# Kernel optimization log

Measured on AMD Instinct MI355X. Metric: run time of the kernel, lower is better.

The kernel has to match this reference:

```python
import jax, jax.numpy as jnp
import numpy as np

B, A, F, D, C = 256, 128, 512, 6, 512  # batch, max_atoms, atom_features, max_degree, conv_width


def setup_inputs() -> dict:
    key = jax.random.key(0)
    k1, k2, k3, k4 = jax.random.split(key, 4)
    atoms = jax.random.normal(k1, (B, A, F), dtype=jnp.float32)
    # neighbour indices in [0, A); pad entries beyond each atom's degree with -1
    neigh = jax.random.randint(k2, (B, A, D), 0, A)
    deg = jax.random.randint(k3, (B, A, 1), 0, D)  # degrees in 0..D-1
    bonds = jnp.where(jnp.arange(D)[None, None, :] < deg, neigh, -1)
    # one Dense(conv_width) per degree: stacked kernels [D, F, C] and biases [D, C]
    W = jax.random.normal(k4, (D, F, C), dtype=jnp.float32) * 0.02
    b = jnp.zeros((D, C), dtype=jnp.float32)
    return {"atoms": atoms, "bonds": bonds, "W": W, "b": b}


def reference(atoms, bonds, W, b):
    d_max = bonds.shape[-1]
    # per-atom degree = count of non -1 neighbour slots  [B, A, 1]
    degrees = jnp.sum(bonds != -1, axis=-1, keepdims=True)
    # shift lookup by 1 so that padded (-1) neighbours index a zero row
    padded = jnp.pad(atoms, ((0, 0), (1, 1), (0, 0)))  # [B, A+2, F]
    idx = bonds + 1  # [B, A, D]
    # per-sample gather of neighbour features -> [B, A, D, F]
    neigh_feats = jax.vmap(lambda ref, i: ref[i])(padded, idx)
    summed = jnp.sum(neigh_feats, axis=2) + atoms  # [B, A, F]
    # apply all degree-specific dense layers, then mask-select by degree
    dense = jnp.einsum('baf,dfc->badc', summed, W) + b  # [B, A, D, C]
    masks = (degrees[..., None] == jnp.arange(d_max).reshape(1, 1, d_max, 1)).astype(dense.dtype)
    return jnp.sum(dense * masks, axis=2)  # [B, A, C]
```

## Files before the change

kernel.cpp:

```cpp
#include <hip/hip_runtime.h>
#include <hip/hip_bf16.h>


#define NB 256
#define NA 128
#define NF 512
#define ND 6
#define NC 512
#define NATOMS (NB * NA)

typedef __attribute__((ext_vector_type(8))) short frag8;
typedef __attribute__((ext_vector_type(4))) float f32x4;

static __device__ inline unsigned short f2bu(float f) {
    __hip_bfloat16 h = __float2bfloat16(f);
    return *reinterpret_cast<unsigned short*>(&h);
}
static __device__ inline unsigned int pack2(float a, float b) {
    return (unsigned int)f2bu(a) | ((unsigned int)f2bu(b) << 16);
}
static __device__ inline void async16(const void* g, void* l) {
    __builtin_amdgcn_global_load_lds(
        (const __attribute__((address_space(1))) void*)g,
        (__attribute__((address_space(3))) void*)l, 16, 0, 0);
}

__global__ void transpose_w(const float* __restrict__ W,
                            __hip_bfloat16* __restrict__ Wt,
                            int* __restrict__ counts) {
    if (blockIdx.x == 0 && blockIdx.y == 0 && blockIdx.z == 0 &&
        threadIdx.y == 0 && threadIdx.x < ND)
        counts[threadIdx.x] = 0;
    __shared__ float t[32][33];
    const int d  = blockIdx.z;
    const int c0 = blockIdx.x * 32;
    const int f0 = blockIdx.y * 32;
    #pragma unroll
    for (int r = 0; r < 32; r += 8)
        t[threadIdx.y + r][threadIdx.x] =
            W[((size_t)(d * NF + f0 + threadIdx.y + r)) * NC + c0 + threadIdx.x];
    __syncthreads();
    #pragma unroll
    for (int r = 0; r < 32; r += 8)
        Wt[((size_t)(d * NC + c0 + threadIdx.y + r)) * NF + f0 + threadIdx.x] =
            __float2bfloat16(t[threadIdx.x][threadIdx.y + r]);
}

__global__ __launch_bounds__(256) void bucket_atoms(
    const int* __restrict__ bonds, int* __restrict__ counts,
    int* __restrict__ bucket) {
    __shared__ int lcnt[ND];
    __shared__ int lbase[ND];
    const int tid = threadIdx.x;
    if (tid < ND) lcnt[tid] = 0;
    __syncthreads();
    int deg[4], loc[4], gg[4];
    #pragma unroll
    for (int i = 0; i < 4; ++i) {
        int g = blockIdx.x * 1024 + i * 256 + tid;
        gg[i] = g;
        int dg = 0;
        #pragma unroll
        for (int j = 0; j < ND; ++j) dg += (bonds[g * ND + j] >= 0);
        deg[i] = dg;
        loc[i] = atomicAdd(&lcnt[dg], 1);
    }
    __syncthreads();
    if (tid < ND) lbase[tid] = atomicAdd(&counts[tid], lcnt[tid]);
    __syncthreads();
    #pragma unroll
    for (int i = 0; i < 4; ++i)
        bucket[deg[i] * NATOMS + lbase[deg[i]] + loc[i]] = gg[i];
}

__global__ __launch_bounds__(256) void sum_neigh(
    const float* __restrict__ atoms, const int* __restrict__ bonds,
    __hip_bfloat16* __restrict__ summed) {
    const int tid  = threadIdx.x;
    const int wave = tid >> 6;
    const int lane = tid & 63;
    const int swz  = (blockIdx.x & 7) * (NATOMS / 4 / 8) + (blockIdx.x >> 3);
    const int g    = swz * 4 + wave;
    const float4* a4 = (const float4*)atoms;

    int   nb[ND];
    float msk[ND];
    #pragma unroll
    for (int j = 0; j < ND; ++j) {
        int n = bonds[g * ND + j];
        msk[j] = (n >= 0) ? 1.0f : 0.0f;
        nb[j]  = (n >= 0) ? n : 0;
    }
    const int rowbase = g & ~(NA - 1);

    float4 s0 = a4[(size_t)g * 128 + lane];
    float4 s1 = a4[(size_t)g * 128 + 64 + lane];
    float4 v0[ND], v1[ND];
    #pragma unroll
    for (int j = 0; j < ND; ++j) {
        const size_t base = (size_t)(rowbase + nb[j]) * 128;
        v0[j] = a4[base + lane];
        v1[j] = a4[base + 64 + lane];
    }
    #pragma unroll
    for (int j = 0; j < ND; ++j) {
        s0.x = fmaf(v0[j].x, msk[j], s0.x); s0.y = fmaf(v0[j].y, msk[j], s0.y);
        s0.z = fmaf(v0[j].z, msk[j], s0.z); s0.w = fmaf(v0[j].w, msk[j], s0.w);
        s1.x = fmaf(v1[j].x, msk[j], s1.x); s1.y = fmaf(v1[j].y, msk[j], s1.y);
        s1.z = fmaf(v1[j].z, msk[j], s1.z); s1.w = fmaf(v1[j].w, msk[j], s1.w);
    }

    uint2 o0, o1;
    o0.x = pack2(s0.x, s0.y); o0.y = pack2(s0.z, s0.w);
    o1.x = pack2(s1.x, s1.y); o1.y = pack2(s1.z, s1.w);
    ((uint2*)summed)[(size_t)g * 128 + lane] = o0;
    ((uint2*)summed)[(size_t)g * 128 + 64 + lane] = o1;
}

__global__ __launch_bounds__(256, 2) void gemm_deg(
    const __hip_bfloat16* __restrict__ summed, const __hip_bfloat16* __restrict__ Wt,
    const float* __restrict__ bias, const int* __restrict__ counts,
    const int* __restrict__ bucket, float* __restrict__ out) {
    const int L  = blockIdx.x + 24 * blockIdx.y;
    const int q  = L >> 3;
    const int p  = ((q >> 2) << 3) + (L & 7);
    const int d  = p % ND;
    const int m0 = (p / ND) * 128;
    const int n0 = (q & 3) * 128;
    const int Md = counts[d];
    if (m0 >= Md) return;

    __shared__ __align__(16) __hip_bfloat16 sA[2][128 * 64];
    __shared__ __align__(16) __hip_bfloat16 sB[2][128 * 64];
    __shared__ int sRows[128];

    const int tid = threadIdx.x;
    if (tid < 128) {
        int r = m0 + tid;
        sRows[tid] = (r < Md) ? bucket[d * NATOMS + r] : -1;
    }
    __syncthreads();

    const int lane = tid & 63;
    const int w    = tid >> 6;
    const int srow = lane >> 3;
    const int seg  = lane & 7;

    const char* smB = (const char*)summed;
    const char* wtB = (const char*)Wt + (size_t)(d * NC + n0) * (NF * 2);
    size_t gA[4];
    int    rowc[4];
    #pragma unroll
    for (int c = 0; c < 4; ++c) {
        rowc[c] = w * 32 + c * 8 + srow;
        int qr = sRows[rowc[c]];
        gA[c] = (size_t)((qr < 0) ? 0 : qr) * (NF * 2);
    }

    const int quad = lane >> 4, l16 = lane & 15;
    const int wy = w >> 1, wx = w & 1;

    f32x4 acc[4][4];
    #pragma unroll
    for (int i = 0; i < 4; ++i)
        #pragma unroll
        for (int j = 0; j < 4; ++j) acc[i][j] = (f32x4)0.0f;

    auto stage = [&](int buf, int kt) {
        const int koff = kt * 128 + seg * 16;
        #pragma unroll
        for (int c = 0; c < 4; ++c) {
            async16(smB + gA[c] + koff, &sA[buf][(w * 32 + c * 8) * 64]);
            async16(wtB + (size_t)rowc[c] * (NF * 2) + koff, &sB[buf][(w * 32 + c * 8) * 64]);
        }
    };
    auto compute = [&](int buf) {
        #pragma unroll
        for (int ks = 0; ks < 64; ks += 32) {
            frag8 aF[4], bF[4];
            #pragma unroll
            for (int i = 0; i < 4; ++i)
                aF[i] = *(const frag8*)&sA[buf][(wy * 64 + i * 16 + l16) * 64 + ks + quad * 8];
            #pragma unroll
            for (int j = 0; j < 4; ++j)
                bF[j] = *(const frag8*)&sB[buf][(wx * 64 + j * 16 + l16) * 64 + ks + quad * 8];
            #pragma unroll
            for (int i = 0; i < 4; ++i)
                #pragma unroll
                for (int j = 0; j < 4; ++j)
                    acc[i][j] = __builtin_amdgcn_mfma_f32_16x16x32_bf16(
                        aF[i], bF[j], acc[i][j], 0, 0, 0);
        }
    };

    stage(0, 0);
    __syncthreads();
    int cur = 0;
    #pragma unroll
    for (int kt = 1; kt < NF / 64; ++kt) {
        stage(cur ^ 1, kt);
        compute(cur);
        __syncthreads();
        cur ^= 1;
    }
    compute(cur);

    #pragma unroll
    for (int j = 0; j < 4; ++j) {
        const int n = n0 + wx * 64 + j * 16 + l16;
        const float bv = bias[d * NC + n];
        #pragma unroll
        for (int i = 0; i < 4; ++i) {
            #pragma unroll
            for (int r = 0; r < 4; ++r) {
                const int tr = wy * 64 + i * 16 + quad * 4 + r;
                const int g  = sRows[tr];
                if (g >= 0)
                    out[(size_t)g * NC + n] = acc[i][j][r] + bv;
            }
        }
    }
}

extern "C" void kernel_launch(void* const* d_in, const int* in_sizes, int n_in,
                              void* d_out, int out_size, void* d_ws, size_t ws_size,
                              hipStream_t stream) {
    const float* atoms = (const float*)d_in[0];
    const int*   bonds = (const int*)d_in[1];
    const float* W     = (const float*)d_in[2];
    const float* bias  = (const float*)d_in[3];
    float* out = (float*)d_out;

    char* ws = (char*)d_ws;
    int* counts = (int*)ws;
    int* bucket = (int*)(ws + 1024);
    __hip_bfloat16* Wt     = (__hip_bfloat16*)(ws + 1024 + 786432);
    __hip_bfloat16* summed = (__hip_bfloat16*)(ws + 1024 + 786432 + 3145728);

    transpose_w<<<dim3(NC / 32, NF / 32, ND), dim3(32, 8), 0, stream>>>(W, Wt, counts);

    bucket_atoms<<<NATOMS / 1024, 256, 0, stream>>>(bonds, counts, bucket);

    sum_neigh<<<NATOMS / 4, 256, 0, stream>>>(atoms, bonds, summed);

    gemm_deg<<<dim3(24, NATOMS / 128), 256, 0, stream>>>(
        summed, Wt, bias, counts, bucket, out);
}
```

Before: 199.1 us.

## Swizzle LDS tiles with XOR and pipeline async loads with partial waitcnt

The async global-to-LDS copies now place each 16-byte segment at an XOR-swizzled position (segment ^ row). The fragment reads apply the matching XOR so that MFMA operand loads avoid LDS bank conflicts. The K-loop drops the full __syncthreads and issues the next stage first, then waits with vmcnt(8) so only the current buffer's loads must land before compute, and raises wave priority during the MFMA section. This overlaps the global loads with compute, but it relies on hand-written waitcnt counts and barrier ordering being correct.

```diff
diff --git a/kernel.cpp b/kernel.cpp
--- a/kernel.cpp
+++ b/kernel.cpp
@@ -156,8 +156,10 @@
         int qr = sRows[rowc[c]];
         gA[c] = (size_t)((qr < 0) ? 0 : qr) * (NF * 2);
     }
+    const int segswz = seg ^ srow;
 
     const int quad = lane >> 4, l16 = lane & 15;
+    const int xr   = l16 & 7;
     const int wy = w >> 1, wx = w & 1;
 
     f32x4 acc[4][4];
@@ -167,7 +169,7 @@
         for (int j = 0; j < 4; ++j) acc[i][j] = (f32x4)0.0f;
 
     auto stage = [&](int buf, int kt) {
-        const int koff = kt * 128 + seg * 16;
+        const int koff = kt * 128 + segswz * 16;
         #pragma unroll
         for (int c = 0; c < 4; ++c) {
             async16(smB + gA[c] + koff, &sA[buf][(w * 32 + c * 8) * 64]);
@@ -176,14 +178,16 @@
     };
     auto compute = [&](int buf) {
         #pragma unroll
-        for (int ks = 0; ks < 64; ks += 32) {
+        for (int ks8 = 0; ks8 < 8; ks8 += 4) {
             frag8 aF[4], bF[4];
             #pragma unroll
             for (int i = 0; i < 4; ++i)
-                aF[i] = *(const frag8*)&sA[buf][(wy * 64 + i * 16 + l16) * 64 + ks + quad * 8];
+                aF[i] = *(const frag8*)&sA[buf][(wy * 64 + i * 16 + l16) * 64 +
+                                                (((ks8 + quad) ^ xr) << 3)];
             #pragma unroll
             for (int j = 0; j < 4; ++j)
-                bF[j] = *(const frag8*)&sB[buf][(wx * 64 + j * 16 + l16) * 64 + ks + quad * 8];
+                bF[j] = *(const frag8*)&sB[buf][(wx * 64 + j * 16 + l16) * 64 +
+                                                (((ks8 + quad) ^ xr) << 3)];
             #pragma unroll
             for (int i = 0; i < 4; ++i)
                 #pragma unroll
@@ -194,16 +198,21 @@
     };
 
     stage(0, 0);
-    __syncthreads();
-    int cur = 0;
     #pragma unroll
     for (int kt = 1; kt < NF / 64; ++kt) {
-        stage(cur ^ 1, kt);
-        compute(cur);
-        __syncthreads();
-        cur ^= 1;
-    }
-    compute(cur);
+        stage(kt & 1, kt);
+        asm volatile("s_waitcnt vmcnt(8)" ::: "memory");
+        __builtin_amdgcn_s_barrier();
+        __builtin_amdgcn_s_setprio(1);
+        compute((kt - 1) & 1);
+        __builtin_amdgcn_s_setprio(0);
+        __builtin_amdgcn_s_barrier();
+    }
+    asm volatile("s_waitcnt vmcnt(0)" ::: "memory");
+    __builtin_amdgcn_s_barrier();
+    __builtin_amdgcn_s_setprio(1);
+    compute((NF / 64 - 1) & 1);
+    __builtin_amdgcn_s_setprio(0);
 
     #pragma unroll
     for (int j = 0; j < 4; ++j) {
```

New measurement: 191.9 us. -3.6%, faster.
